# Optimization experiments

Hardware: AMD Instinct MI355X
Metric: run time of the kernel (lower is better)

## Reference

```python
import jax, jax.numpy as jnp
import numpy as np

NUM_HEADS = 16


def setup_inputs() -> dict:
    key = jax.random.key(0)
    ks = jax.random.split(key, 6)
    dim = 1024
    B, N = 4, 4096
    s = 1.0 / np.sqrt(dim)
    return {
        "x": jax.random.normal(ks[0], (B, N, dim), dtype=jnp.float32),
        "Wq": jax.random.normal(ks[1], (dim, dim), dtype=jnp.float32) * s,
        "Wk": jax.random.normal(ks[2], (dim, dim), dtype=jnp.float32) * s,
        "Wv": jax.random.normal(ks[3], (dim, dim), dtype=jnp.float32) * s,
        "Wo": jax.random.normal(ks[4], (dim, dim), dtype=jnp.float32) * s,
        "bo": jnp.zeros((dim,), dtype=jnp.float32),
    }


def reference(x, Wq, Wk, Wv, Wo, bo):
    # STAtten (linear attention) branch, no SNN, dropout = 0 (identity in eval).
    B, N, C = x.shape
    H = NUM_HEADS
    D = C // H
    scale = D ** (-0.5)

    def heads(W):
        # torch nn.Linear: y = x @ W.T ; then [B,N,H,D] -> [B,H,N,D]
        y = jnp.einsum('bnc,oc->bno', x, W)
        return y.reshape(B, N, H, D).transpose(0, 2, 1, 3)

    q = heads(Wq)
    k = heads(Wk)
    v = heads(Wv)

    kv = jnp.einsum('bhnd,bhne->bhde', k, v) * scale  # [B,H,D,D]
    out = jnp.einsum('bhnd,bhde->bhne', q, kv)        # [B,H,N,D]

    out = out.transpose(0, 2, 1, 3).reshape(B, N, C)
    return jnp.einsum('bnc,oc->bno', out, Wo) + bo
```

## Files before the change

### kernel.cpp

```cpp
#include <hip/hip_runtime.h>
#include <hip/hip_bf16.h>
#include <math.h>

typedef __hip_bfloat16 bf16;
typedef float f32x4 __attribute__((ext_vector_type(4)));
typedef short s16x8 __attribute__((ext_vector_type(8)));

typedef const __attribute__((address_space(1))) void* as1cvp;
typedef __attribute__((address_space(3))) void* as3vp;

__device__ __forceinline__ unsigned short f2bf(float f) {
  unsigned u = __float_as_uint(f);
  u += 0x7FFFu + ((u >> 16) & 1u);
  return (unsigned short)(u >> 16);
}
__device__ __forceinline__ float bf2f(unsigned short s) {
  return __uint_as_float(((unsigned)s) << 16);
}

__device__ __forceinline__ void gpu_barrier() {
  asm volatile("" ::: "memory");
  __builtin_amdgcn_s_barrier();
  asm volatile("" ::: "memory");
}

__device__ __forceinline__ void tri_decode(int xt, int* ti_out, int* tj_out) {
  int tj = (int)((sqrtf(8.0f * (float)xt + 1.0f) - 1.0f) * 0.5f);
  int tri = tj * (tj + 1) / 2;
  if (xt < tri) { --tj; tri = tj * (tj + 1) / 2; }
  else if (xt >= tri + tj + 1) { ++tj; tri = tj * (tj + 1) / 2; }
  *ti_out = xt - tri;
  *tj_out = tj;
}

__global__ __launch_bounds__(256) void cast_transpose(const float* __restrict__ x,
                                                      unsigned short* __restrict__ xb,
                                                      unsigned short* __restrict__ xT) {
  __shared__ unsigned short tl[128 * 136];
  const int n0 = blockIdx.x * 128, d0 = blockIdx.y * 128, b = blockIdx.z;
  const int t = threadIdx.x;

  const int rr0 = t >> 4;
  const int u   = t & 15;
  const int dd  = u * 8;
#pragma unroll
  for (int it = 0; it < 8; ++it) {
    const int rr = rr0 + it * 16;
    const float* src = x + ((long)(b * 4096 + n0 + rr)) * 1024 + d0 + dd;
    f32x4 v0 = *(const f32x4*)src;
    f32x4 v1 = *(const f32x4*)(src + 4);
    s16x8 o;
    o[0] = (short)f2bf(v0[0]); o[1] = (short)f2bf(v0[1]);
    o[2] = (short)f2bf(v0[2]); o[3] = (short)f2bf(v0[3]);
    o[4] = (short)f2bf(v1[0]); o[5] = (short)f2bf(v1[1]);
    o[6] = (short)f2bf(v1[2]); o[7] = (short)f2bf(v1[3]);
    *(s16x8*)&xb[((long)(b * 4096 + n0 + rr)) * 1024 + d0 + dd] = o;
    const int phys = u ^ (rr >> 3);
    *(s16x8*)&tl[rr * 136 + phys * 8] = o;
  }
  __syncthreads();

  const int nblk = t & 15, dblk = t >> 4;
  s16x8 row[8];
#pragma unroll
  for (int j = 0; j < 8; ++j) {
    const int n = nblk * 8 + j;
    const int phys = dblk ^ nblk;
    row[j] = *(const s16x8*)&tl[n * 136 + phys * 8];
  }
#pragma unroll
  for (int c = 0; c < 8; ++c) {
    s16x8 col;
#pragma unroll
    for (int j = 0; j < 8; ++j) col[j] = row[j][c];
    *(s16x8*)&xT[((long)(b * 1024 + d0 + dblk * 8 + c)) * 4096 + n0 + nblk * 8] = col;
  }
}

__global__ __launch_bounds__(256) void cast_weights(const float* __restrict__ Wq,
                                                    const float* __restrict__ Wk,
                                                    const float* __restrict__ Wv,
                                                    const float* __restrict__ Wo,
                                                    unsigned short* __restrict__ Wkb,
                                                    unsigned short* __restrict__ Wvb,
                                                    unsigned short* __restrict__ Wqb,
                                                    unsigned short* __restrict__ Wob) {
  const int i = blockIdx.x * 256 + threadIdx.x;
  const int seg = blockIdx.y;
  const long flat = (long)i * 8;
  const float* src = (seg == 0) ? Wk : (seg == 1) ? Wv : (seg == 2) ? Wq : Wo;
  f32x4 v0 = *(const f32x4*)&src[flat];
  f32x4 v1 = *(const f32x4*)&src[flat + 4];
  s16x8 o;
  o[0] = (short)f2bf(v0[0]); o[1] = (short)f2bf(v0[1]);
  o[2] = (short)f2bf(v0[2]); o[3] = (short)f2bf(v0[3]);
  o[4] = (short)f2bf(v1[0]); o[5] = (short)f2bf(v1[1]);
  o[6] = (short)f2bf(v1[2]); o[7] = (short)f2bf(v1[3]);
  unsigned short* dst = (seg == 0) ? Wkb : (seg == 1) ? Wvb : (seg == 2) ? Wqb : Wob;
  *(s16x8*)&dst[flat] = o;
}

template<bool OUTF32>
__global__ __launch_bounds__(512, 2) void gemm256(
    const bf16* __restrict__ A, int lda, long aOffY, long aOffZ,
    const bf16* __restrict__ Bt, int ldb, long btOffY, long btOffZ,
    void* __restrict__ Cv, int ldc, long cOffY, long cOffZ,
    const float* __restrict__ bias, int K, int NtN, int gridmode)
{
  __shared__ char lds[131072];

  const int Nx = gridDim.x, Ny = gridDim.y;
  const int lin = blockIdx.x + Nx * (blockIdx.y + Ny * blockIdx.z);
  const int tot = Nx * Ny * gridDim.z;
  const int swz = (lin & 7) * (tot >> 3) + (lin >> 3);
  const int xt = swz % Nx;
  const int r2 = swz / Nx;
  const int y = r2 % Ny, z = r2 / Ny;
  int ti, tj;
  if (gridmode == 1) {
    ti = (int)((0x3221110000ULL >> (4 * xt)) & 15);
    tj = (int)((0x3323213210ULL >> (4 * xt)) & 15);
  } else { ti = xt / NtN; tj = xt % NtN; }
  const int bm = ti * 256, bn = tj * 256;

  A  += (long)z * aOffZ + (long)y * aOffY;
  Bt += (long)z * btOffZ + (long)y * btOffY;

  const int tid  = threadIdx.x;
  const int wid  = tid >> 6;
  const int lane = tid & 63;
  const int wm = wid >> 2;
  const int wn = wid & 3;
  const int frow = lane & 15;
  const int fkb  = (lane >> 4) << 4;
  const unsigned xorv = (unsigned)((lane & 7) << 4);

  const int q0 = (tid * 16) ^ (((tid >> 3) & 7) << 4);
  const int q1 = (8192 + tid * 16) ^ (((tid >> 3) & 7) << 4);
  const int srow0 = q0 >> 7, scol0 = (q0 & 127) >> 1;
  const int srow1 = q1 >> 7, scol1 = (q1 & 127) >> 1;
  const bf16* ag0 = A  + (long)(bm + srow0) * lda + scol0;
  const bf16* ag1 = A  + (long)(bm + srow1) * lda + scol1;
  const bf16* bg0 = Bt + (long)(bn + srow0) * ldb + scol0;
  const bf16* bg1 = Bt + (long)(bn + srow1) * ldb + scol1;

#define STAGE_A(buf, half, kk) do {                                                  \
    __builtin_amdgcn_global_load_lds((as1cvp)(ag0 + (long)(half)*128*lda + (kk)),    \
        (as3vp)(lds + (buf)*32768 + (half)*16384 + wid*1024), 16, 0, 0);             \
    __builtin_amdgcn_global_load_lds((as1cvp)(ag1 + (long)(half)*128*lda + (kk)),    \
        (as3vp)(lds + (buf)*32768 + (half)*16384 + 8192 + wid*1024), 16, 0, 0);      \
  } while (0)
#define STAGE_B(buf, half, kk) do {                                                  \
    __builtin_amdgcn_global_load_lds((as1cvp)(bg0 + (long)(half)*128*ldb + (kk)),    \
        (as3vp)(lds + 65536 + (buf)*32768 + (half)*16384 + wid*1024), 16, 0, 0);     \
    __builtin_amdgcn_global_load_lds((as1cvp)(bg1 + (long)(half)*128*ldb + (kk)),    \
        (as3vp)(lds + 65536 + (buf)*32768 + (half)*16384 + 8192 + wid*1024), 16, 0, 0); \
  } while (0)

  const unsigned paBase = (unsigned)((wm * 64 + frow) * 128 + fkb);
  const unsigned pbBase = (unsigned)(((wn & 1) * 64 + frow) * 128 + fkb);
  const unsigned bHalf  = (unsigned)((wn >> 1) * 16384);

#define RD_A(dst, cur, Mh, mi, kh)                                                   \
  dst = *(const s16x8*)(lds + (cur)*32768 + (Mh)*16384 +                             \
                        ((paBase + (mi)*2048u + (kh)*64u) ^ xorv))
#define RD_B(dst, cur, nj, kh)                                                       \
  dst = *(const s16x8*)(lds + 65536 + (cur)*32768 + bHalf +                          \
                        ((pbBase + (nj)*2048u + (kh)*64u) ^ xorv))

#define MFMA16(base, bb)                                                             \
  __builtin_amdgcn_s_setprio(1);                                                     \
  _Pragma("unroll")                                                                  \
  for (int mi = 0; mi < 4; ++mi)                                                     \
    _Pragma("unroll")                                                                \
    for (int nj = 0; nj < 4; ++nj)                                                   \
      acc[(base) + mi][nj] = __builtin_amdgcn_mfma_f32_16x16x32_bf16(                \
          a[mi], bb[nj], acc[(base) + mi][nj], 0, 0, 0);                             \
  __builtin_amdgcn_s_setprio(0);

#define LGKM0 asm volatile("s_waitcnt lgkmcnt(0)" ::: "memory")
#define VM8   asm volatile("s_waitcnt vmcnt(8)" ::: "memory")

  f32x4 acc[8][4] = {};
  s16x8 a[4], b0[4], b1[4];
  const int NT = K >> 6;

  STAGE_A(0, 0, 0); STAGE_B(0, 0, 0); STAGE_B(0, 1, 0);
  STAGE_A(0, 1, 0);
  {
    const int kk = (NT > 1) ? 64 : 0;
    STAGE_A(1, 0, kk); STAGE_B(1, 0, kk); STAGE_B(1, 1, kk);
  }
  VM8;
  gpu_barrier();

  for (int t = 0; t < NT; ++t) {
    const int cur = t & 1, nxt = cur ^ 1;
    const int k1 = ((t + 1 < NT) ? (t + 1) : 0) * 64;
    const int k2 = ((t + 2 < NT) ? (t + 2) : 0) * 64;

#pragma unroll
    for (int mi = 0; mi < 4; ++mi) RD_A(a[mi], cur, 0, mi, 0);
#pragma unroll
    for (int nj = 0; nj < 4; ++nj) RD_B(b0[nj], cur, nj, 0);
    STAGE_A(nxt, 1, k1);
    gpu_barrier(); LGKM0;
    MFMA16(0, b0)
    gpu_barrier();

#pragma unroll
    for (int mi = 0; mi < 4; ++mi) RD_A(a[mi], cur, 0, mi, 1);
#pragma unroll
    for (int nj = 0; nj < 4; ++nj) RD_B(b1[nj], cur, nj, 1);
    gpu_barrier(); LGKM0;
    MFMA16(0, b1)
    VM8;
    gpu_barrier();

#pragma unroll
    for (int mi = 0; mi < 4; ++mi) RD_A(a[mi], cur, 1, mi, 0);
    STAGE_A(cur, 0, k2); STAGE_B(cur, 0, k2); STAGE_B(cur, 1, k2);
    gpu_barrier(); LGKM0;
    MFMA16(4, b0)
    gpu_barrier();

#pragma unroll
    for (int mi = 0; mi < 4; ++mi) RD_A(a[mi], cur, 1, mi, 1);
    gpu_barrier(); LGKM0;
    MFMA16(4, b1)
    VM8;
    gpu_barrier();
  }

  asm volatile("s_waitcnt vmcnt(0)" ::: "memory");

  const int crow0 = bm + wm * 64 + (lane >> 4) * 4;
  const int ccol0 = bn + wn * 64 + (lane & 15);
  if (OUTF32) {
    float* C = (float*)Cv + (long)z * cOffZ + (long)y * cOffY;
    float bs[4];
#pragma unroll
    for (int j = 0; j < 4; ++j) bs[j] = bias ? bias[ccol0 + j * 16] : 0.0f;
#pragma unroll
    for (int i = 0; i < 8; ++i) {
      const int row = crow0 + (i >> 2) * 128 + (i & 3) * 16;
#pragma unroll
      for (int j = 0; j < 4; ++j) {
        const int col = ccol0 + j * 16;
#pragma unroll
        for (int r = 0; r < 4; ++r)
          C[(long)(row + r) * ldc + col] = acc[i][j][r] + bs[j];
      }
    }
  } else {
    unsigned short* C = (unsigned short*)Cv + (long)z * cOffZ + (long)y * cOffY;
#pragma unroll
    for (int i = 0; i < 8; ++i) {
      const int row = crow0 + (i >> 2) * 128 + (i & 3) * 16;
#pragma unroll
      for (int j = 0; j < 4; ++j) {
        const int col = ccol0 + j * 16;
#pragma unroll
        for (int r = 0; r < 4; ++r)
          C[(long)(row + r) * ldc + col] = f2bf(acc[i][j][r]);
      }
    }
  }
#undef STAGE_A
#undef STAGE_B
#undef RD_A
#undef RD_B
#undef MFMA16
#undef LGKM0
#undef VM8
}

template<int MODE>
__global__ __launch_bounds__(256) void gemm128(
    const bf16* __restrict__ A0, const bf16* __restrict__ B0,
    void* __restrict__ Cv, const float* __restrict__ bias)
{
  __shared__ char lds[65536];

  const int Nx = gridDim.x;
  const int lin = blockIdx.x + Nx * blockIdx.y;
  const int tot = Nx * gridDim.y;
  const int swz = (lin & 7) * (tot >> 3) + (lin >> 3);
  const int xt = swz % Nx, yy = swz / Nx;

  const int lda = 1024;
  const int ldb = 1024;
  const int K   = 1024;
  const int bm = (xt >> 3) * 128, bn = (xt & 7) * 128;
  const bf16* A  = A0;
  const bf16* Bt = B0 + (long)yy * 1048576L;

  const int tid  = threadIdx.x;
  const int wid  = tid >> 6;
  const int lane = tid & 63;
  const int wr = (wid >> 1) * 64, wc = (wid & 1) * 64;
  const int frow = lane & 15;
  const int fkb  = (lane >> 4) << 4;
  const unsigned xorv = (unsigned)((lane & 7) << 4);

  const int q0 = (tid * 16) ^ (((tid >> 3) & 7) << 4);
  const int srow0 = q0 >> 7, scol0 = (q0 & 127) >> 1;
  const bf16* ag = A  + (long)(bm + srow0) * lda + scol0;
  const bf16* bg = Bt + (long)(bn + srow0) * ldb + scol0;

#define STG128(buf, kk) do {                                                         \
    _Pragma("unroll")                                                                \
    for (int i = 0; i < 4; ++i) {                                                    \
      __builtin_amdgcn_global_load_lds((as1cvp)(ag + (long)i * 32 * lda + (kk)),     \
          (as3vp)(lds + (buf) * 16384 + i * 4096 + tid * 16), 16, 0, 0);             \
      __builtin_amdgcn_global_load_lds((as1cvp)(bg + (long)i * 32 * ldb + (kk)),     \
          (as3vp)(lds + 32768 + (buf) * 16384 + i * 4096 + tid * 16), 16, 0, 0);     \
    }                                                                                \
  } while (0)

  const unsigned paB = (unsigned)((wr + frow) * 128 + fkb);
  const unsigned pbB = (unsigned)((wc + frow) * 128 + fkb);

  f32x4 acc[4][4] = {};
  const int NT = K >> 6;

  STG128(0, 0);
  asm volatile("s_waitcnt vmcnt(0)" ::: "memory");
  gpu_barrier();

  for (int t = 0; t < NT; ++t) {
    const int cur = t & 1;
    if (t + 1 < NT) STG128(cur ^ 1, (t + 1) * 64);
    s16x8 a[4][2], b[4][2];
#pragma unroll
    for (int mi = 0; mi < 4; ++mi)
#pragma unroll
      for (int kh = 0; kh < 2; ++kh)
        a[mi][kh] = *(const s16x8*)(lds + cur * 16384 +
                                    ((paB + mi * 2048u + kh * 64u) ^ xorv));
#pragma unroll
    for (int nj = 0; nj < 4; ++nj)
#pragma unroll
      for (int kh = 0; kh < 2; ++kh)
        b[nj][kh] = *(const s16x8*)(lds + 32768 + cur * 16384 +
                                    ((pbB + nj * 2048u + kh * 64u) ^ xorv));
    asm volatile("s_waitcnt lgkmcnt(0)" ::: "memory");
#pragma unroll
    for (int mi = 0; mi < 4; ++mi)
#pragma unroll
      for (int nj = 0; nj < 4; ++nj) {
        acc[mi][nj] = __builtin_amdgcn_mfma_f32_16x16x32_bf16(a[mi][0], b[nj][0], acc[mi][nj], 0, 0, 0);
        acc[mi][nj] = __builtin_amdgcn_mfma_f32_16x16x32_bf16(a[mi][1], b[nj][1], acc[mi][nj], 0, 0, 0);
      }
    asm volatile("s_waitcnt vmcnt(0)" ::: "memory");
    gpu_barrier();
  }

  const int r0 = wr + (lane >> 4) * 4;
  const int c0t = wc + (lane & 15);
  unsigned short* C = (unsigned short*)Cv + (long)yy * 1048576;
#pragma unroll
  for (int mi = 0; mi < 4; ++mi)
#pragma unroll
    for (int nj = 0; nj < 4; ++nj)
#pragma unroll
      for (int r = 0; r < 4; ++r)
        C[(long)(bm + r0 + mi * 16 + r) * 1024 + bn + c0t + nj * 16] =
            f2bf(acc[mi][nj][r]);
#undef STG128
}

template<int OUTMODE>
__global__ __launch_bounds__(256) void gemm64(
    const bf16* __restrict__ A, int lda, long aOffZ,
    const bf16* __restrict__ Bt, int ldb, long btOffZ,
    void* __restrict__ Cv, int ldc, long cOffZ, int loOff,
    int K, int NtN, int dmode, int ksplit)
{
  __shared__ char lds[32768];

  const int Nx = gridDim.x;
  const int lin = blockIdx.x + Nx * blockIdx.y;
  const int tot = Nx * gridDim.y;
  const int swz = (lin & 7) * (tot >> 3) + (lin >> 3);
  const int xt = swz % Nx, y = swz / Nx;
  const int zb = y / ksplit, zs = y % ksplit;
  int ti, tj;
  if (dmode == 2)      { tri_decode(xt, &ti, &tj); }
  else if (dmode == 1) { ti = xt; tj = xt; }
  else                 { ti = xt / NtN; tj = xt % NtN; }
  const int bm = ti * 64, bn = tj * 64;

  A  += (long)zb * aOffZ + (long)zs * K;
  Bt += (long)zb * btOffZ + (long)zs * K;

  const int tid  = threadIdx.x;
  const int wid  = tid >> 6;
  const int lane = tid & 63;
  const int wr = (wid >> 1) * 32, wc = (wid & 1) * 32;
  const int frow = lane & 15;
  const int fkb  = (lane >> 4) << 4;
  const unsigned xorv = (unsigned)((lane & 7) << 4);

  const int q0 = (tid * 16) ^ (((tid >> 3) & 7) << 4);
  const int q1 = (4096 + tid * 16) ^ (((tid >> 3) & 7) << 4);
  const int srow0 = q0 >> 7, scol0 = (q0 & 127) >> 1;
  const int srow1 = q1 >> 7, scol1 = (q1 & 127) >> 1;
  const bf16* ag0 = A  + (long)(bm + srow0) * lda + scol0;
  const bf16* ag1 = A  + (long)(bm + srow1) * lda + scol1;
  const bf16* bg0 = Bt + (long)(bn + srow0) * ldb + scol0;
  const bf16* bg1 = Bt + (long)(bn + srow1) * ldb + scol1;

#define STAGE64(buf, kk) do {                                                        \
    __builtin_amdgcn_global_load_lds((as1cvp)(ag0 + (kk)),                           \
        (as3vp)(lds + (buf)*8192 + wid*1024), 16, 0, 0);                             \
    __builtin_amdgcn_global_load_lds((as1cvp)(ag1 + (kk)),                           \
        (as3vp)(lds + (buf)*8192 + 4096 + wid*1024), 16, 0, 0);                      \
    __builtin_amdgcn_global_load_lds((as1cvp)(bg0 + (kk)),                           \
        (as3vp)(lds + 16384 + (buf)*8192 + wid*1024), 16, 0, 0);                     \
    __builtin_amdgcn_global_load_lds((as1cvp)(bg1 + (kk)),                           \
        (as3vp)(lds + 16384 + (buf)*8192 + 4096 + wid*1024), 16, 0, 0);              \
  } while (0)

  const unsigned paB = (unsigned)((wr + frow) * 128 + fkb);
  const unsigned pbB = (unsigned)((wc + frow) * 128 + fkb);

  f32x4 acc[2][2] = {};
  const int NT = K >> 6;

  STAGE64(0, 0);
  asm volatile("s_waitcnt vmcnt(0)" ::: "memory");
  gpu_barrier();

  for (int t = 0; t < NT; ++t) {
    const int cur = t & 1;
    if (t + 1 < NT) STAGE64(cur ^ 1, (t + 1) * 64);
    s16x8 a[2][2], b[2][2];
#pragma unroll
    for (int mi = 0; mi < 2; ++mi)
#pragma unroll
      for (int kh = 0; kh < 2; ++kh)
        a[mi][kh] = *(const s16x8*)(lds + cur * 8192 +
                                    ((paB + mi * 2048u + kh * 64u) ^ xorv));
#pragma unroll
    for (int nj = 0; nj < 2; ++nj)
#pragma unroll
      for (int kh = 0; kh < 2; ++kh)
        b[nj][kh] = *(const s16x8*)(lds + 16384 + cur * 8192 +
                                    ((pbB + nj * 2048u + kh * 64u) ^ xorv));
    asm volatile("s_waitcnt lgkmcnt(0)" ::: "memory");
#pragma unroll
    for (int mi = 0; mi < 2; ++mi)
#pragma unroll
      for (int nj = 0; nj < 2; ++nj) {
        acc[mi][nj] = __builtin_amdgcn_mfma_f32_16x16x32_bf16(a[mi][0], b[nj][0], acc[mi][nj], 0, 0, 0);
        acc[mi][nj] = __builtin_amdgcn_mfma_f32_16x16x32_bf16(a[mi][1], b[nj][1], acc[mi][nj], 0, 0, 0);
      }
    asm volatile("s_waitcnt vmcnt(0)" ::: "memory");
    gpu_barrier();
  }

  const int r0 = wr + (lane >> 4) * 4;
  const int c0 = wc + (lane & 15);
  if (OUTMODE == 1) {
    float* C = (float*)Cv + (long)y * cOffZ + (long)xt * 4096;
#pragma unroll
    for (int mi = 0; mi < 2; ++mi)
#pragma unroll
      for (int nj = 0; nj < 2; ++nj)
#pragma unroll
        for (int r = 0; r < 4; ++r)
          C[(r0 + mi * 16 + r) * 64 + c0 + nj * 16] = acc[mi][nj][r];
  } else if (OUTMODE == 3) {
    unsigned short* C = (unsigned short*)Cv + (long)y * cOffZ;
#pragma unroll
    for (int mi = 0; mi < 2; ++mi)
#pragma unroll
      for (int nj = 0; nj < 2; ++nj)
#pragma unroll
        for (int r = 0; r < 4; ++r) {
          const unsigned short h = f2bf(acc[mi][nj][r]);
          const int R = bm + r0 + mi * 16 + r;
          const int Cc = bn + c0 + nj * 16;
          C[(long)R * 1024 + Cc] = h;
          if (ti != tj) C[(long)Cc * 1024 + R] = h;
        }
  } else {
    unsigned short* C = (unsigned short*)Cv + (long)y * cOffZ;
#pragma unroll
    for (int mi = 0; mi < 2; ++mi)
#pragma unroll
      for (int nj = 0; nj < 2; ++nj)
#pragma unroll
        for (int r = 0; r < 4; ++r) {
          const float v = acc[mi][nj][r];
          const unsigned short h = f2bf(v);
          const long idx = (long)(bm + r0 + mi * 16 + r) * ldc + bn + c0 + nj * 16;
          C[idx] = h;
          if (OUTMODE == 2) C[idx + loOff] = f2bf(v - bf2f(h));
        }
  }
#undef STAGE64
}

__global__ __launch_bounds__(256) void yt_kernel(const float* __restrict__ Up,
                                                 const unsigned short* __restrict__ Wqb,
                                                 unsigned short* __restrict__ Yt) {
  __shared__ float Ul[64 * 64];
  __shared__ float Wql[64 * 68];
  const int cblk = blockIdx.x, h = blockIdx.y, z = blockIdx.z;
  const int t = threadIdx.x;

  {
    const int d = t >> 2, e0 = (t & 3) * 16;
#pragma unroll
    for (int q = 0; q < 4; ++q) {
      f32x4 s = {};
#pragma unroll
      for (int sp = 0; sp < 4; ++sp) {
        f32x4 v = *(const f32x4*)&Up[((long)(z * 4 + sp) * 16 + h) * 4096 + d * 64 + e0 + q * 4];
#pragma unroll
        for (int j = 0; j < 4; ++j) s[j] += v[j];
      }
      *(f32x4*)&Ul[d * 64 + e0 + q * 4] = s;
    }
    const unsigned short* wp = Wqb + (long)(h * 64 + d) * 1024 + cblk * 64 + e0;
#pragma unroll
    for (int q = 0; q < 2; ++q) {
      s16x8 w = *(const s16x8*)&wp[q * 8];
#pragma unroll
      for (int j = 0; j < 8; ++j) Wql[d * 68 + e0 + q * 8 + j] = bf2f((unsigned short)w[j]);
    }
  }
  __syncthreads();

  const int jc = t >> 2, e0 = (t & 3) * 16;
  f32x4 acc[4] = {};
  for (int d = 0; d < 64; ++d) {
    const float w = Wql[d * 68 + jc];
    const float* ur = &Ul[d * 64 + e0];
#pragma unroll
    for (int q = 0; q < 4; ++q) {
      f32x4 u4 = *(const f32x4*)&ur[q * 4];
#pragma unroll
      for (int j = 0; j < 4; ++j) acc[q][j] += w * u4[j];
    }
  }
  unsigned short* yp = Yt + (long)z * 1048576 + (long)(cblk * 64 + jc) * 1024 + h * 64 + e0;
#pragma unroll
  for (int q = 0; q < 4; ++q)
#pragma unroll
    for (int j = 0; j < 4; ++j) yp[q * 4 + j] = f2bf(acc[q][j] * 0.125f);
}

extern "C" void kernel_launch(void* const* d_in, const int* in_sizes, int n_in,
                              void* d_out, int out_size, void* d_ws, size_t ws_size,
                              hipStream_t stream) {
  const float* x  = (const float*)d_in[0];
  const float* Wq = (const float*)d_in[1];
  const float* Wk = (const float*)d_in[2];
  const float* Wv = (const float*)d_in[3];
  const float* Wo = (const float*)d_in[4];
  const float* bo = (const float*)d_in[5];
  float* out = (float*)d_out;

  char* ws = (char*)d_ws;
  unsigned short* xb  = (unsigned short*)(ws);
  unsigned short* xT  = (unsigned short*)(ws + 33554432);
  unsigned short* Wkb = (unsigned short*)(ws + 67108864);
  unsigned short* Wvb = (unsigned short*)(ws + 71303168);
  unsigned short* Wqb = (unsigned short*)(ws + 75497472);
  unsigned short* Wob = (unsigned short*)(ws + 77594624);
  unsigned short* Gb  = (unsigned short*)(ws + 79691776);
  unsigned short* T   = (unsigned short*)(ws + 88080384);
  float*          Up  = (float*)         (ws + 96468992);
  unsigned short* Yt  = (unsigned short*)(ws + 113246208);
  unsigned short* R   = (unsigned short*)(ws + 121634816);

  cast_transpose<<<dim3(32, 8, 4), 256, 0, stream>>>(x, xb, xT);
  cast_weights<<<dim3(512, 4), 256, 0, stream>>>(Wq, Wk, Wv, Wo, Wkb, Wvb, Wqb, Wob);

  gemm64<3><<<dim3(136, 4), 256, 0, stream>>>(
      (const bf16*)xT, 4096, 4194304L, (const bf16*)xT, 4096, 4194304L,
      (void*)Gb, 1024, 1048576L, 0, 4096, 1, 2, 1);

  gemm128<3><<<dim3(64, 4), 256, 0, stream>>>(
      (const bf16*)Wkb, (const bf16*)Gb, (void*)T, nullptr);

  gemm64<1><<<dim3(16, 16), 256, 0, stream>>>(
      (const bf16*)T, 1024, 1048576L, (const bf16*)Wvb, 1024, 0L,
      (void*)Up, 64, 65536L, 0, 256, 1, 1, 4);

  yt_kernel<<<dim3(16, 16, 4), 256, 0, stream>>>(Up, Wqb, Yt);

  gemm128<3><<<dim3(64, 4), 256, 0, stream>>>(
      (const bf16*)Wob, (const bf16*)Yt, (void*)R, nullptr);

  gemm256<true><<<dim3(64, 1, 4), 512, 0, stream>>>(
      (const bf16*)xb, 1024, 0L, 4194304L,
      (const bf16*)R, 1024, 0L, 1048576L,
      (void*)out, 1024, 0L, 4194304L,
      bo, 1024, 4, 0);
}
```

Measured before the change: 166.5 us.

## Split-K the 1024x1024 GEMMs with bf16 partials and fuse cast kernels

Merges the input cast/transpose and weight-cast kernels into a single launch using extra z-blocks. The two 1024-deep gemm128 launches become a two-way split-K that writes bf16 partial products to a scratch buffer, followed by a small reduction kernel. This doubles the block count to fill more CUs, at the cost of an extra launch, additional memory traffic, and an extra bf16 rounding of the partials. The diff introduces MODE 4 for gemm128, and its epilogue for writing the partials is not visible.

```diff
diff --git a/kernel.cpp b/kernel.cpp
--- a/kernel.cpp
+++ b/kernel.cpp
@@ -33,13 +33,37 @@
   *tj_out = tj;
 }
 
-__global__ __launch_bounds__(256) void cast_transpose(const float* __restrict__ x,
-                                                      unsigned short* __restrict__ xb,
-                                                      unsigned short* __restrict__ xT) {
+__global__ __launch_bounds__(256) void cast_fused(const float* __restrict__ x,
+                                                  unsigned short* __restrict__ xb,
+                                                  unsigned short* __restrict__ xT,
+                                                  const float* __restrict__ Wq,
+                                                  const float* __restrict__ Wk,
+                                                  const float* __restrict__ Wv,
+                                                  const float* __restrict__ Wo,
+                                                  unsigned short* __restrict__ Wkb,
+                                                  unsigned short* __restrict__ Wvb,
+                                                  unsigned short* __restrict__ Wqb,
+                                                  unsigned short* __restrict__ Wob) {
+  const int t = threadIdx.x;
+  if (blockIdx.z >= 4) {
+    const int zz = blockIdx.z - 4;
+    const int seg = zz >> 1;
+    const int blk = (zz & 1) * 256 + blockIdx.y * 32 + blockIdx.x;
+    const long flat = ((long)blk * 256 + t) * 8;
+    const float* src = (seg == 0) ? Wk : (seg == 1) ? Wv : (seg == 2) ? Wq : Wo;
+    f32x4 v0 = *(const f32x4*)&src[flat];
+    f32x4 v1 = *(const f32x4*)&src[flat + 4];
+    s16x8 o;
+    o[0] = (short)f2bf(v0[0]); o[1] = (short)f2bf(v0[1]);
+    o[2] = (short)f2bf(v0[2]); o[3] = (short)f2bf(v0[3]);
+    o[4] = (short)f2bf(v1[0]); o[5] = (short)f2bf(v1[1]);
+    o[6] = (short)f2bf(v1[2]); o[7] = (short)f2bf(v1[3]);
+    unsigned short* dst = (seg == 0) ? Wkb : (seg == 1) ? Wvb : (seg == 2) ? Wqb : Wob;
+    *(s16x8*)&dst[flat] = o;
+    return;
+  }
   __shared__ unsigned short tl[128 * 136];
   const int n0 = blockIdx.x * 128, d0 = blockIdx.y * 128, b = blockIdx.z;
-  const int t = threadIdx.x;
-
   const int rr0 = t >> 4;
   const int u   = t & 15;
   const int dd  = u * 8;
@@ -77,27 +101,16 @@
   }
 }
 
-__global__ __launch_bounds__(256) void cast_weights(const float* __restrict__ Wq,
-                                                    const float* __restrict__ Wk,
-                                                    const float* __restrict__ Wv,
-                                                    const float* __restrict__ Wo,
-                                                    unsigned short* __restrict__ Wkb,
-                                                    unsigned short* __restrict__ Wvb,
-                                                    unsigned short* __restrict__ Wqb,
-                                                    unsigned short* __restrict__ Wob) {
-  const int i = blockIdx.x * 256 + threadIdx.x;
-  const int seg = blockIdx.y;
-  const long flat = (long)i * 8;
-  const float* src = (seg == 0) ? Wk : (seg == 1) ? Wv : (seg == 2) ? Wq : Wo;
-  f32x4 v0 = *(const f32x4*)&src[flat];
-  f32x4 v1 = *(const f32x4*)&src[flat + 4];
+__global__ __launch_bounds__(256) void red2(const unsigned short* __restrict__ P,
+                                            unsigned short* __restrict__ Out) {
+  const long i = ((long)blockIdx.x * 256 + threadIdx.x) * 8;
+  s16x8 a = *(const s16x8*)&P[i];
+  s16x8 b = *(const s16x8*)&P[i + 4194304];
   s16x8 o;
-  o[0] = (short)f2bf(v0[0]); o[1] = (short)f2bf(v0[1]);
-  o[2] = (short)f2bf(v0[2]); o[3] = (short)f2bf(v0[3]);
-  o[4] = (short)f2bf(v1[0]); o[5] = (short)f2bf(v1[1]);
-  o[6] = (short)f2bf(v1[2]); o[7] = (short)f2bf(v1[3]);
-  unsigned short* dst = (seg == 0) ? Wkb : (seg == 1) ? Wvb : (seg == 2) ? Wqb : Wob;
-  *(s16x8*)&dst[flat] = o;
+#pragma unroll
+  for (int j = 0; j < 8; ++j)
+    o[j] = (short)f2bf(bf2f((unsigned short)a[j]) + bf2f((unsigned short)b[j]));
+  *(s16x8*)&Out[i] = o;
 }
 
 template<bool OUTF32>
@@ -278,7 +291,7 @@
 template<int MODE>
 __global__ __launch_bounds__(256) void gemm128(
     const bf16* __restrict__ A0, const bf16* __restrict__ B0,
-    void* __restrict__ Cv, const float* __restrict__ bias)
+    void* __restrict__ Cv, int Kp)
 {
   __shared__ char lds[65536];
 
@@ -290,10 +303,10 @@
 
   const int lda = 1024;
   const int ldb = 1024;
-  const int K   = 1024;
   const int bm = (xt >> 3) * 128, bn = (xt & 7) * 128;
-  const bf16* A  = A0;
-  const bf16* Bt = B0 + (long)yy * 1048576L;
+  const int batch = yy & 3, split = yy >> 2;
+  const bf16* A  = A0 + split * 512;
+  const bf16* Bt = B0 + (long)batch * 1048576L + split * 512;
 
   const int tid  = threadIdx.x;
   const int wid  = tid >> 6;
@@ -322,7 +335,7 @@
   const unsigned pbB = (unsigned)((wc + frow) * 128 + fkb);
 
   f32x4 acc[4][4] = {};
-  const int NT = K >> 6;
+  const int NT = Kp >> 6;
 
   STG128(0, 0);
   asm volatile("s_waitcnt vmcnt(0)" ::: "memory");
@@ -573,19 +586,21 @@
   unsigned short* Wob = (unsigned short*)(ws + 77594624);
   unsigned short* Gb  = (unsigned short*)(ws + 79691776);
   unsigned short* T   = (unsigned short*)(ws + 88080384);
-  float*          Up  = (float*)         (ws + 96468992);
+  unsigned short* Pp  = (unsigned short*)(ws + 96468992);
   unsigned short* Yt  = (unsigned short*)(ws + 113246208);
   unsigned short* R   = (unsigned short*)(ws + 121634816);
-
-  cast_transpose<<<dim3(32, 8, 4), 256, 0, stream>>>(x, xb, xT);
-  cast_weights<<<dim3(512, 4), 256, 0, stream>>>(Wq, Wk, Wv, Wo, Wkb, Wvb, Wqb, Wob);
+  float*          Up  = (float*)         (ws + 130023424);
+
+  cast_fused<<<dim3(32, 8, 12), 256, 0, stream>>>(
+      x, xb, xT, Wq, Wk, Wv, Wo, Wkb, Wvb, Wqb, Wob);
 
   gemm64<3><<<dim3(136, 4), 256, 0, stream>>>(
       (const bf16*)xT, 4096, 4194304L, (const bf16*)xT, 4096, 4194304L,
       (void*)Gb, 1024, 1048576L, 0, 4096, 1, 2, 1);
 
-  gemm128<3><<<dim3(64, 4), 256, 0, stream>>>(
-      (const bf16*)Wkb, (const bf16*)Gb, (void*)T, nullptr);
+  gemm128<4><<<dim3(64, 8), 256, 0, stream>>>(
+      (const bf16*)Wkb, (const bf16*)Gb, (void*)Pp, 512);
+  red2<<<2048, 256, 0, stream>>>(Pp, T);
 
   gemm64<1><<<dim3(16, 16), 256, 0, stream>>>(
       (const bf16*)T, 1024, 1048576L, (const bf16*)Wvb, 1024, 0L,
@@ -593,8 +608,9 @@
 
   yt_kernel<<<dim3(16, 16, 4), 256, 0, stream>>>(Up, Wqb, Yt);
 
-  gemm128<3><<<dim3(64, 4), 256, 0, stream>>>(
-      (const bf16*)Wob, (const bf16*)Yt, (void*)R, nullptr);
+  gemm128<4><<<dim3(64, 8), 256, 0, stream>>>(
+      (const bf16*)Wob, (const bf16*)Yt, (void*)Pp, 512);
+  red2<<<2048, 256, 0, stream>>>(Pp, R);
 
   gemm256<true><<<dim3(64, 1, 4), 512, 0, stream>>>(
       (const bf16*)xb, 1024, 0L, 4194304L,
```

After: 173.3 us. +4.1%, slower.
